# Optimization experiments

Measured on AMD Instinct MI355X. Metric: run time of the kernel, lower is better.

Reference implementation:

```python
import jax, jax.numpy as jnp
import numpy as np

NQ = 4  # n_qubits_per_head


def _apply_ry(state, theta, q):
    # state: (N, 2,2,2,2) real amplitudes; theta: (N,) per-element angle; wire q
    st = jnp.moveaxis(state, 1 + q, -1)
    c = jnp.cos(0.5 * theta).reshape(-1, 1, 1, 1)
    s = jnp.sin(0.5 * theta).reshape(-1, 1, 1, 1)
    a0, a1 = st[..., 0], st[..., 1]
    st = jnp.stack([c * a0 - s * a1, s * a0 + c * a1], axis=-1)
    return jnp.moveaxis(st, -1, 1 + q)


def _apply_cnot(state, ctrl, tgt):
    st = jnp.moveaxis(state, (1 + ctrl, 1 + tgt), (-2, -1))
    st = jnp.stack([st[..., 0, :], st[..., 1, ::-1]], axis=-2)
    return jnp.moveaxis(st, (-2, -1), (1 + ctrl, 1 + tgt))


def _quantum_circuit(x_in, par):
    # x_in: (N, NQ) data angles; par: (N, L, NQ) variational angles (per head, tiled)
    N = x_in.shape[0]
    L = par.shape[1]
    state = jnp.zeros((N, 2, 2, 2, 2), x_in.dtype).at[:, 0, 0, 0, 0].set(1.0)
    for l in range(L):
        for q in range(NQ):
            state = _apply_ry(state, par[:, l, q], q)
        for q in range(NQ - 1):
            state = _apply_cnot(state, q, q + 1)
        state = _apply_cnot(state, NQ - 1, 0)
    for q in range(NQ):
        state = _apply_ry(state, x_in[:, q], q)
    p = state * state  # probabilities (real amplitudes: only RY/CNOT gates)
    zs = []
    for q in range(NQ):
        st = jnp.moveaxis(p, 1 + q, -1)
        zs.append(jnp.sum(st[..., 0], axis=(1, 2, 3)) - jnp.sum(st[..., 1], axis=(1, 2, 3)))
    return jnp.stack(zs, axis=-1)  # (N, NQ)


def setup_inputs() -> dict:
    key = jax.random.key(0)
    ks = jax.random.split(key, 6)
    B, T, E, H, L = 4, 2048, 1024, 16, 2
    scale = 1.0 / np.sqrt(E)
    x = jax.random.normal(ks[0], (B, T, E), dtype=jnp.float32)
    Wq = jax.random.normal(ks[1], (E, E), dtype=jnp.float32) * scale
    Wk = jax.random.normal(ks[2], (E, E), dtype=jnp.float32) * scale
    Wv = jax.random.normal(ks[3], (E, E), dtype=jnp.float32) * scale
    Wo = jax.random.normal(ks[4], (E, E), dtype=jnp.float32) * scale
    qparams = jax.random.normal(ks[5], (H, L, NQ), dtype=jnp.float32)
    return {"x": x, "Wq": Wq, "Wk": Wk, "Wv": Wv, "Wo": Wo, "qparams": qparams}


def reference(x, Wq, Wk, Wv, Wo, qparams):
    B, T, E = x.shape
    H, L, _ = qparams.shape
    hd = E // H
    q = x @ Wq.T
    k = x @ Wk.T
    v = x @ Wv.T
    # NOTE: original scales by sqrt(embed_dim), not sqrt(head_dim)
    scores = jnp.einsum('bte,bse->bts', q, k) / jnp.sqrt(jnp.asarray(E, x.dtype))
    w = jax.nn.softmax(scores, axis=-1)
    out = jnp.einsum('bts,bse->bte', w, v)
    oh = out.reshape(B, T, H, hd)
    N = B * T * H
    xin = oh[..., :NQ].reshape(N, NQ)
    par = jnp.broadcast_to(qparams[None, None], (B, T, H, L, NQ)).reshape(N, L, NQ)
    z = _quantum_circuit(xin, par)  # (N, NQ)
    zfull = jnp.concatenate([z, jnp.zeros((N, hd - NQ), x.dtype)], axis=-1)
    return zfull.reshape(B, T, E) @ Wo.T
```

## Files before the change

### kernel.cpp

```cpp
#include <hip/hip_runtime.h>
#include <hip/hip_fp16.h>

typedef _Float16 half_t;
typedef __attribute__((ext_vector_type(4))) _Float16 half4;
typedef __attribute__((ext_vector_type(8))) _Float16 half8;
typedef __attribute__((ext_vector_type(4))) float floatx4;

__device__ __forceinline__ void async_copy16(const void* src, void* dst_lds) {
  __builtin_amdgcn_global_load_lds(
      (__attribute__((address_space(1))) void*)src,
      (__attribute__((address_space(3))) void*)dst_lds, 16, 0, 0);
}

__global__ __launch_bounds__(512, 2) void gemm_nt_256(
    const half_t* __restrict__ A, const half_t* __restrict__ B,
    half_t* __restrict__ C,
    int lda, int ldb, int ldc, int kIters,
    long sAz2, long sBz2, long sCz2, float scale)
{
  __shared__ __align__(16) half_t sm[2][2][256 * 64];

  const int tid  = threadIdx.x;
  const int wave = tid >> 6, lane = tid & 63;
  const int wm = wave >> 2, wn = wave & 3;
  const int er = lane >> 4, ec = lane & 15;
  const int sw = ec & 7;

  const long z = blockIdx.z;
  const half_t* Ab = A + (long)blockIdx.x * 256 * lda + z * sAz2;
  const half_t* Bb = B + (long)blockIdx.y * 256 * ldb + z * sBz2;

  const int srow = tid >> 3;
  const int skq  = (tid & 7) ^ (srow & 7);

  floatx4 acc[2][2][4][2];
  #pragma unroll
  for (int a = 0; a < 2; a++)
    #pragma unroll
    for (int b = 0; b < 2; b++)
      #pragma unroll
      for (int i = 0; i < 4; i++)
        #pragma unroll
        for (int j = 0; j < 2; j++)
          acc[a][b][i][j] = (floatx4){0.f, 0.f, 0.f, 0.f};

#define STAGE_A(bb, hf, kt) do {                                              \
    const half_t* Ak_ = Ab + (long)(kt) * 64;                                 \
    _Pragma("unroll")                                                         \
    for (int r_ = 0; r_ < 2; r_++) {                                          \
      int lrow_ = r_ * 64 + srow;                                             \
      async_copy16(Ak_ + (long)((hf) * 128 + lrow_) * lda + skq * 8,          \
                   &sm[(bb)][0][(hf) * 8192 + (r_ * 512 + wave * 64) * 8]);   \
    } } while (0)

#define STAGE_B(bb, hf, kt) do {                                              \
    const half_t* Bk_ = Bb + (long)(kt) * 64;                                 \
    _Pragma("unroll")                                                         \
    for (int r_ = 0; r_ < 2; r_++) {                                          \
      int lrow_ = r_ * 64 + srow;                                             \
      async_copy16(Bk_ + (long)((hf) * 128 + lrow_) * ldb + skq * 8,          \
                   &sm[(bb)][1][(hf) * 8192 + (r_ * 512 + wave * 64) * 8]);   \
    } } while (0)

#define DS_A(DST, BB, MH) do {                                                \
    _Pragma("unroll")                                                         \
    for (int ii = 0; ii < 4; ii++) {                                          \
      int row_ = (MH) * 128 + wm * 64 + ii * 16 + ec;                         \
      _Pragma("unroll")                                                       \
      for (int ks = 0; ks < 2; ks++)                                          \
        DST[ii][ks] = *(const half8*)                                         \
            &sm[BB][0][row_ * 64 + (((ks * 4 + er) ^ sw) * 8)];               \
    } } while (0)

#define DS_B(DST, BB, NH) do {                                                \
    _Pragma("unroll")                                                         \
    for (int jj = 0; jj < 2; jj++) {                                          \
      int row_ = (NH) * 128 + wn * 32 + jj * 16 + ec;                         \
      _Pragma("unroll")                                                       \
      for (int ks = 0; ks < 2; ks++)                                          \
        DST[jj][ks] = *(const half8*)                                         \
            &sm[BB][1][row_ * 64 + (((ks * 4 + er) ^ sw) * 8)];               \
    } } while (0)

#define MFMA_Q(AF, BF, MH, NH) do {                                           \
    __builtin_amdgcn_s_setprio(1);                                            \
    _Pragma("unroll")                                                         \
    for (int ks = 0; ks < 2; ks++)                                            \
      _Pragma("unroll")                                                       \
      for (int ii = 0; ii < 4; ii++)                                          \
        _Pragma("unroll")                                                     \
        for (int jj = 0; jj < 2; jj++)                                        \
          acc[MH][NH][ii][jj] = __builtin_amdgcn_mfma_f32_16x16x32_f16(       \
              AF[ii][ks], BF[jj][ks], acc[MH][NH][ii][jj], 0, 0, 0);          \
    __builtin_amdgcn_s_setprio(0);                                            \
  } while (0)

#define BAR() __builtin_amdgcn_s_barrier()
#define LGKM0() do { asm volatile("s_waitcnt lgkmcnt(0)" ::: "memory");       \
                     __builtin_amdgcn_sched_barrier(0); } while (0)
#define VMW(N) asm volatile("s_waitcnt vmcnt(" #N ")" ::: "memory")

  half8 afX[4][2], bfX[2][2], bfY[2][2];
  int cur = 0;
  const int nt = kIters;

  STAGE_A(0, 0, 0); STAGE_B(0, 0, 0); STAGE_B(0, 1, 0); STAGE_A(0, 1, 0);
  VMW(4);
  BAR();

  for (int n = 0; n < nt; ++n) {
    const int hasNext = (n + 1 < nt);
    DS_A(afX, cur, 0);
    DS_B(bfX, cur, 0);
    if (hasNext) STAGE_A(cur ^ 1, 0, n + 1);
    BAR(); LGKM0();
    MFMA_Q(afX, bfX, 0, 0);
    if (hasNext) { VMW(4); } else { VMW(0); }
    BAR();
    DS_B(bfY, cur, 1);
    if (hasNext) STAGE_B(cur ^ 1, 0, n + 1);
    BAR(); LGKM0();
    MFMA_Q(afX, bfY, 0, 1);
    if (hasNext) VMW(4);
    BAR();
    DS_A(afX, cur, 1);
    if (hasNext) STAGE_B(cur ^ 1, 1, n + 1);
    BAR(); LGKM0();
    MFMA_Q(afX, bfY, 1, 1);
    BAR();
    if (hasNext) STAGE_A(cur ^ 1, 1, n + 1);
    MFMA_Q(afX, bfX, 1, 0);
    if (hasNext) VMW(4);
    BAR();
    cur ^= 1;
  }

#undef STAGE_A
#undef STAGE_B
#undef DS_A
#undef DS_B
#undef MFMA_Q
#undef BAR
#undef LGKM0
#undef VMW

  const long rowBase = (long)blockIdx.x * 256;
  const long colBase = (long)blockIdx.y * 256;
  half_t* Cz = C + z * sCz2;
  #pragma unroll
  for (int mh = 0; mh < 2; mh++)
    #pragma unroll
    for (int nh = 0; nh < 2; nh++)
      #pragma unroll
      for (int ii = 0; ii < 4; ii++)
        #pragma unroll
        for (int jj = 0; jj < 2; jj++)
          #pragma unroll
          for (int r = 0; r < 4; r++) {
            long row = rowBase + mh * 128 + wm * 64 + ii * 16 + er * 4 + r;
            long col = colBase + nh * 128 + wn * 32 + jj * 16 + ec;
            Cz[row * (long)ldc + col] =
                (_Float16)(acc[mh][nh][ii][jj][r] * scale);
          }
}

template<int BN, int EPI>
__global__ __launch_bounds__(256) void gemm_nt(
    const half_t* __restrict__ A, const half_t* __restrict__ B,
    void* __restrict__ Cout,
    int lda, int ldb, int ldc, int kIters, int zShift,
    long sAz1, long sBz1, long sCz1,
    long sAz2, long sBz2, long sCz2, float scale,
    const float* __restrict__ qab)
{
  constexpr int BM = 128;
  constexpr int WN = BN / 2;
  constexpr int AN = WN / 16;
  constexpr int RA = BM * 8 / 256;
  constexpr int RB = BN * 8 / 256;
  __shared__ __align__(16) half_t lA[BM * 64];
  __shared__ __align__(16) half_t lB[BN * 64];

  const int tid  = threadIdx.x;
  const int wave = tid >> 6, lane = tid & 63;
  const int wm = wave >> 1, wn = wave & 1;
  const int er = lane >> 4, ec = lane & 15;
  const int sw = ec & 7;

  const long z = blockIdx.z;
  const long z2 = z >> zShift;
  const long z1 = z - (z2 << zShift);
  const half_t* Ab = A + (long)blockIdx.x * BM * lda + z1 * sAz1 + z2 * sAz2;
  const half_t* Bb = B + (long)blockIdx.y * BN * ldb + z1 * sBz1 + z2 * sBz2;
  const long cz = z1 * sCz1 + z2 * sCz2;

  floatx4 acc[4][AN];
  #pragma unroll
  for (int i = 0; i < 4; i++)
    #pragma unroll
    for (int j = 0; j < AN; j++)
      acc[i][j] = (floatx4){0.f, 0.f, 0.f, 0.f};

  for (int ks = 0; ks < kIters; ++ks) {
    const half_t* Ak = Ab + ks * 64;
    const half_t* Bk = Bb + ks * 64;
    #pragma unroll
    for (int r = 0; r < RA; r++) {
      int s = r * 256 + tid;
      int row = s >> 3;
      int kq = (s & 7) ^ (row & 7);
      async_copy16(Ak + (long)row * lda + kq * 8,
                   &lA[(r * 256 + wave * 64) * 8]);
    }
    #pragma unroll
    for (int r = 0; r < RB; r++) {
      int s = r * 256 + tid;
      int row = s >> 3;
      int kq = (s & 7) ^ (row & 7);
      async_copy16(Bk + (long)row * ldb + kq * 8,
                   &lB[(r * 256 + wave * 64) * 8]);
    }
    __syncthreads();

    #pragma unroll
    for (int h = 0; h < 2; h++) {
      half8 af[4], bfv[AN];
      #pragma unroll
      for (int i = 0; i < 4; i++) {
        int row = wm * 64 + i * 16 + ec;
        af[i] = *(const half8*)&lA[row * 64 + (((h * 4 + er) ^ sw) * 8)];
      }
      #pragma unroll
      for (int j = 0; j < AN; j++) {
        int row = wn * WN + j * 16 + ec;
        bfv[j] = *(const half8*)&lB[row * 64 + (((h * 4 + er) ^ sw) * 8)];
      }
      #pragma unroll
      for (int i = 0; i < 4; i++)
        #pragma unroll
        for (int j = 0; j < AN; j++)
          acc[i][j] = __builtin_amdgcn_mfma_f32_16x16x32_f16(
              af[i], bfv[j], acc[i][j], 0, 0, 0);
    }
    __syncthreads();
  }

  const long rowBase = (long)blockIdx.x * BM + wm * 64;
  const long colBase = (long)blockIdx.y * BN + wn * WN;
  #pragma unroll
  for (int i = 0; i < 4; i++)
    #pragma unroll
    for (int j = 0; j < AN; j++)
      #pragma unroll
      for (int r = 0; r < 4; r++) {
        long row = rowBase + i * 16 + er * 4 + r;
        long col = colBase + j * 16 + ec;
        float v = acc[i][j][r];
        if constexpr (EPI == 0) {
          ((half_t*)Cout)[cz + row * (long)ldc + col] = (_Float16)(v * scale);
        } else if constexpr (EPI == 1) {
          ((half_t*)Cout)[cz + col * (long)ldc + row] = (_Float16)v;
        } else if constexpr (EPI == 2) {
          ((float*)Cout)[cz + row * (long)ldc + col] = v * scale;
        } else if constexpr (EPI == 4) {
          ((float*)Cout)[cz + col * (long)ldc + row] = v;
        } else {
          float za = qab[2 * (int)col], zb = qab[2 * (int)col + 1];
          float zv = za * cosf(v) + zb * sinf(v);
          ((half_t*)Cout)[cz + row * (long)ldc + col] = (_Float16)zv;
        }
      }
}

__global__ __launch_bounds__(256) void pv_softmax(
    const half_t* __restrict__ S, const half_t* __restrict__ V,
    float* __restrict__ Op, float* __restrict__ Lp, int kIters)
{
  __shared__ __align__(16) half_t lA[128 * 64];
  __shared__ __align__(16) half_t lB[64 * 64];

  const int tid  = threadIdx.x;
  const int wave = tid >> 6, lane = tid & 63;
  const int wm = wave >> 1, wn = wave & 1;
  const int er = lane >> 4, ec = lane & 15;
  const int sw = ec & 7;

  const long z = blockIdx.z;
  const long z2 = z >> 2;
  const long z1 = z & 3;
  const half_t* Ab = S + (long)blockIdx.x * 128 * 2048
                       + z1 * ((long)2048 * 2048) + z2 * 512;
  const half_t* Bb = V + z1 * 2048 + z2 * 512;

  floatx4 acc[4][2];
  #pragma unroll
  for (int i = 0; i < 4; i++)
    #pragma unroll
    for (int j = 0; j < 2; j++)
      acc[i][j] = (floatx4){0.f, 0.f, 0.f, 0.f};
  float lsum[4] = {0.f, 0.f, 0.f, 0.f};

  for (int ks = 0; ks < kIters; ++ks) {
    const half_t* Ak = Ab + ks * 64;
    const half_t* Bk = Bb + ks * 64;
    #pragma unroll
    for (int r = 0; r < 4; r++) {
      int s = r * 256 + tid;
      int row = s >> 3;
      int kq = (s & 7) ^ (row & 7);
      async_copy16(Ak + (long)row * 2048 + kq * 8,
                   &lA[(r * 256 + wave * 64) * 8]);
    }
    #pragma unroll
    for (int r = 0; r < 2; r++) {
      int s = r * 256 + tid;
      int row = s >> 3;
      int kq = (s & 7) ^ (row & 7);
      async_copy16(Bk + (long)row * 8192 + kq * 8,
                   &lB[(r * 256 + wave * 64) * 8]);
    }
    __syncthreads();

    #pragma unroll
    for (int h = 0; h < 2; h++) {
      half8 af[4], bfv[2];
      #pragma unroll
      for (int i = 0; i < 4; i++) {
        int row = wm * 64 + i * 16 + ec;
        half8 a = *(const half8*)&lA[row * 64 + (((h * 4 + er) ^ sw) * 8)];
        #pragma unroll
        for (int k = 0; k < 8; k++) {
          float e = __expf((float)a[k]);
          _Float16 ph = (_Float16)e;
          a[k] = ph;
          lsum[i] += (float)ph;
        }
        af[i] = a;
      }
      #pragma unroll
      for (int j = 0; j < 2; j++) {
        int row = wn * 32 + j * 16 + ec;
        bfv[j] = *(const half8*)&lB[row * 64 + (((h * 4 + er) ^ sw) * 8)];
      }
      #pragma unroll
      for (int i = 0; i < 4; i++)
        #pragma unroll
        for (int j = 0; j < 2; j++)
          acc[i][j] = __builtin_amdgcn_mfma_f32_16x16x32_f16(
              af[i], bfv[j], acc[i][j], 0, 0, 0);
    }
    __syncthreads();
  }

  const long zo = z2 * ((long)8192 * 64) + z1 * ((long)2048 * 64);
  const long rowBase = (long)blockIdx.x * 128 + wm * 64;
  #pragma unroll
  for (int i = 0; i < 4; i++)
    #pragma unroll
    for (int j = 0; j < 2; j++)
      #pragma unroll
      for (int r = 0; r < 4; r++) {
        long row = rowBase + i * 16 + er * 4 + r;
        long col = wn * 32 + j * 16 + ec;
        Op[zo + row * 64 + col] = acc[i][j][r];
      }

  const long lb = z2 * 8192 + z1 * 2048 + (long)blockIdx.x * 128 + wm * 64;
  #pragma unroll
  for (int i = 0; i < 4; i++) {
    float v = lsum[i];
    v += __shfl_xor(v, 16);
    v += __shfl_xor(v, 32);
    if (wn == 0 && er == 0) Lp[lb + i * 16 + ec] = v;
  }
}

__global__ __launch_bounds__(256) void v4_reduce(const float* __restrict__ P,
                                                 half_t* __restrict__ O)
{
  const long CH = (long)64 * 8192;
  long i = ((long)blockIdx.x * 256 + threadIdx.x) * 4;
  float4 a = *(const float4*)(P + i);
  float4 b = *(const float4*)(P + i + CH);
  float4 c = *(const float4*)(P + i + 2 * CH);
  float4 d = *(const float4*)(P + i + 3 * CH);
  half4 o;
  o[0] = (_Float16)(a.x + b.x + c.x + d.x);
  o[1] = (_Float16)(a.y + b.y + c.y + d.y);
  o[2] = (_Float16)(a.z + b.z + c.z + d.z);
  o[3] = (_Float16)(a.w + b.w + c.w + d.w);
  *(half4*)(O + i) = o;
}

__global__ __launch_bounds__(256) void z_reduce_quantum(
    const float* __restrict__ P, const float* __restrict__ Lp,
    const float* __restrict__ qab, half_t* __restrict__ O)
{
  const long CH = (long)8192 * 64;
  long i = ((long)blockIdx.x * 256 + threadIdx.x) * 4;
  long t = i >> 6;
  float4 a = *(const float4*)(P + i);
  float4 b = *(const float4*)(P + i + CH);
  float4 c = *(const float4*)(P + i + 2 * CH);
  float4 d = *(const float4*)(P + i + 3 * CH);
  float l = Lp[t] + Lp[8192 + t] + Lp[2 * 8192 + t] + Lp[3 * 8192 + t];
  float inv = 1.f / l;
  float s[4] = {(a.x + b.x + c.x + d.x) * inv, (a.y + b.y + c.y + d.y) * inv,
                (a.z + b.z + c.z + d.z) * inv, (a.w + b.w + c.w + d.w) * inv};
  int c0 = (int)(i & 63);
  half4 o;
  #pragma unroll
  for (int j = 0; j < 4; j++) {
    float za = qab[2 * (c0 + j)], zb = qab[2 * (c0 + j) + 1];
    o[j] = (_Float16)(za * cosf(s[j]) + zb * sinf(s[j]));
  }
  *(half4*)(O + i) = o;
}

__global__ __launch_bounds__(256) void softmax_rows(half_t* __restrict__ S,
                                                    int ld)
{
  const long row = blockIdx.x;
  half8* sp = (half8*)(S + row * (long)ld);
  const int t = threadIdx.x;
  const int wave = t >> 6, lane = t & 63;
  half8 hv = sp[t];
  float e[8];
  #pragma unroll
  for (int k = 0; k < 8; k++) e[k] = (float)hv[k];
  float m = e[0];
  #pragma unroll
  for (int k = 1; k < 8; k++) m = fmaxf(m, e[k]);
  #pragma unroll
  for (int o = 32; o > 0; o >>= 1) m = fmaxf(m, __shfl_xor(m, o));
  __shared__ float rmax[4], rsum[4];
  if (lane == 0) rmax[wave] = m;
  __syncthreads();
  m = fmaxf(fmaxf(rmax[0], rmax[1]), fmaxf(rmax[2], rmax[3]));
  float s = 0.f;
  #pragma unroll
  for (int k = 0; k < 8; k++) { e[k] = expf(e[k] - m); s += e[k]; }
  #pragma unroll
  for (int o = 32; o > 0; o >>= 1) s += __shfl_xor(s, o);
  if (lane == 0) rsum[wave] = s;
  __syncthreads();
  float inv = 1.f / (rsum[0] + rsum[1] + rsum[2] + rsum[3]);
  half8 o8;
  #pragma unroll
  for (int k = 0; k < 8; k++) o8[k] = (_Float16)(e[k] * inv);
  sp[t] = o8;
}

__global__ __launch_bounds__(256) void prep_all(
    const float* __restrict__ x,  const float* __restrict__ Wq,
    const float* __restrict__ Wk, const float* __restrict__ Wv,
    const float* __restrict__ Wo, const float* __restrict__ qp, int L,
    half_t* __restrict__ xh, half_t* __restrict__ Wqk,
    half_t* __restrict__ Wv4, half_t* __restrict__ Wos,
    float* __restrict__ qab)
{
  const int bid = blockIdx.x;
  if (bid < 4096) {
    long i = ((long)bid * 256 + threadIdx.x) * 8;
    float4 a = *(const float4*)(x + i);
    float4 b = *(const float4*)(x + i + 4);
    half8 h = {(_Float16)a.x, (_Float16)a.y, (_Float16)a.z, (_Float16)a.w,
               (_Float16)b.x, (_Float16)b.y, (_Float16)b.z, (_Float16)b.w};
    *(half8*)(xh + i) = h;
  } else if (bid < 5120) {
    long i = ((long)(bid - 4096) * 256 + threadIdx.x) * 8;
    int r = (int)(i >> 10);
    int e = (int)(i & 1023);
    const float* src = (r < 1024 ? Wq + (long)r * 1024
                                 : Wk + (long)(r - 1024) * 1024) + e;
    float4 a = *(const float4*)src;
    float4 b = *(const float4*)(src + 4);
    half8 h = {(_Float16)a.x, (_Float16)a.y, (_Float16)a.z, (_Float16)a.w,
               (_Float16)b.x, (_Float16)b.y, (_Float16)b.z, (_Float16)b.w};
    *(half8*)(Wqk + i) = h;
  } else if (bid < 5152) {
    long i = ((long)(bid - 5120) * 256 + threadIdx.x) * 8;
    int c = (int)(i >> 10);
    int e = (int)(i & 1023);
    const float* src = Wv + (long)(((c >> 2) << 6) | (c & 3)) * 1024 + e;
    float4 a = *(const float4*)src;
    float4 b = *(const float4*)(src + 4);
    half8 h = {(_Float16)a.x, (_Float16)a.y, (_Float16)a.z, (_Float16)a.w,
               (_Float16)b.x, (_Float16)b.y, (_Float16)b.z, (_Float16)b.w};
    *(half8*)(Wv4 + i) = h;
  } else if (bid < 5408) {
    int idx = (bid - 5152) * 256 + threadIdx.x;
    int e = idx >> 6, c = idx & 63;
    Wos[idx] = (_Float16)Wo[(long)e * 1024 + (((c >> 2) << 6) | (c & 3))];
  } else {
    int h = threadIdx.x;
    if (h >= 16) return;
    float st[16];
    #pragma unroll
    for (int i = 0; i < 16; i++) st[i] = 0.f;
    st[0] = 1.f;
    for (int l = 0; l < L; l++) {
      #pragma unroll
      for (int q = 0; q < 4; q++) {
        float th = qp[(h * L + l) * 4 + q];
        float c = cosf(0.5f * th), s = sinf(0.5f * th);
        int mq = 8 >> q;
        #pragma unroll
        for (int i = 0; i < 16; i++) {
          if ((i & mq) == 0) {
            float a0 = st[i], a1 = st[i | mq];
            st[i]      = c * a0 - s * a1;
            st[i | mq] = s * a0 + c * a1;
          }
        }
      }
      const int cm[4] = {8, 4, 2, 1};
      const int tm[4] = {4, 2, 1, 8};
      #pragma unroll
      for (int p = 0; p < 4; p++) {
        int mc = cm[p], mt = tm[p];
        #pragma unroll
        for (int i = 0; i < 16; i++) {
          if ((i & mc) != 0 && (i & mt) == 0) {
            float tv = st[i]; st[i] = st[i | mt]; st[i | mt] = tv;
          }
        }
      }
    }
    #pragma unroll
    for (int q = 0; q < 4; q++) {
      int mq = 8 >> q;
      float zc = 0.f, xc = 0.f;
      #pragma unroll
      for (int i = 0; i < 16; i++) {
        float p2 = st[i] * st[i];
        zc += ((i & mq) == 0) ? p2 : -p2;
        if ((i & mq) == 0) xc += st[i] * st[i | mq];
      }
      qab[(h * 4 + q) * 2 + 0] = zc;
      qab[(h * 4 + q) * 2 + 1] = -2.f * xc;
    }
  }
}

extern "C" void kernel_launch(void* const* d_in, const int* in_sizes, int n_in,
                              void* d_out, int out_size, void* d_ws, size_t ws_size,
                              hipStream_t stream)
{
  const float* x  = (const float*)d_in[0];
  const float* Wq = (const float*)d_in[1];
  const float* Wk = (const float*)d_in[2];
  const float* Wv = (const float*)d_in[3];
  const float* Wo = (const float*)d_in[4];
  const float* qp = (const float*)d_in[5];
  const int L = in_sizes[5] / 64;
  float* out = (float*)d_out;

  char* w = (char*)d_ws;
  size_t off = 0;
  auto alloc = [&](size_t bytes) -> void* {
    void* p = w + off;
    off = (off + bytes + 255) & ~(size_t)255;
    return p;
  };
  float*  qab  = (float*)alloc(512);
  half_t* xh   = (half_t*)alloc((size_t)8192 * 1024 * 2);
  half_t* Wqk  = (half_t*)alloc((size_t)2048 * 1024 * 2);
  half_t* Wv4  = (half_t*)alloc((size_t)64 * 1024 * 2);
  half_t* Wos  = (half_t*)alloc((size_t)1024 * 64 * 2);
  half_t* V4th = (half_t*)alloc((size_t)64 * 8192 * 2);
  half_t* Z4   = (half_t*)alloc((size_t)8192 * 64 * 2);
  float*  Lp   = (float*)alloc((size_t)4 * 8192 * 4);

  half_t* QKb = (half_t*)d_out;

  int tier = (ws_size >= off + (size_t)8192 * 2048 * 2 + 256) ? 0 : 1;
  const size_t Sn = (tier == 0) ? (size_t)8192 * 2048 : (size_t)2048 * 2048;
  half_t* S = (half_t*)alloc(Sn * 2);

  prep_all<<<dim3(5409), dim3(256), 0, stream>>>(
      x, Wq, Wk, Wv, Wo, qp, L, xh, Wqk, Wv4, Wos, qab);

  gemm_nt_256<<<dim3(32, 8, 1), 512, 0, stream>>>(
      xh, Wqk, QKb, 1024, 1024, 2048, 16, 0, 0, 0, 1.f);

  if (tier == 0) {
    float* V4p = (float*)S;
    gemm_nt<64, 4><<<dim3(64, 1, 4), 256, 0, stream>>>(
        xh, Wv4, V4p, 1024, 1024, 8192, 4, 0,
        0, 0, 0, 256, 256, (long)64 * 8192, 1.f, nullptr);
    v4_reduce<<<dim3(512), dim3(256), 0, stream>>>(V4p, V4th);

    gemm_nt_256<<<dim3(8, 8, 4), 512, 0, stream>>>(
        QKb, QKb + 1024, S, 2048, 2048, 2048, 16,
        (long)2048 * 2048, (long)2048 * 2048, (long)2048 * 2048, 0.03125f);

    float* Zp = (float*)d_out;
    pv_softmax<<<dim3(16, 1, 16), 256, 0, stream>>>(S, V4th, Zp, Lp, 8);
    z_reduce_quantum<<<dim3(512), dim3(256), 0, stream>>>(Zp, Lp, qab, Z4);
  } else {
    gemm_nt<64, 1><<<dim3(64, 1, 1), 256, 0, stream>>>(
        xh, Wv4, V4th, 1024, 1024, 8192, 16, 0,
        0, 0, 0, 0, 0, 0, 1.f, nullptr);
    for (int b = 0; b < 4; b++) {
      const long q0 = (long)b * 2048;
      gemm_nt<128, 0><<<dim3(16, 16, 1), 256, 0, stream>>>(
          QKb + q0 * 2048, QKb + 1024 + q0 * 2048, S,
          2048, 2048, 2048, 16, 0, 0, 0, 0, 0, 0, 0, 0.03125f, nullptr);
      softmax_rows<<<dim3(2048), dim3(256), 0, stream>>>(S, 2048);
      gemm_nt<64, 5><<<dim3(16, 1, 1), 256, 0, stream>>>(
          S, V4th + q0, Z4 + q0 * 64, 2048, 8192, 64, 32, 0,
          0, 0, 0, 0, 0, 0, 1.f, qab);
    }
  }

  gemm_nt<128, 2><<<dim3(64, 8, 1), 256, 0, stream>>>(
      Z4, Wos, out, 64, 64, 1024, 1, 0,
      0, 0, 0, 0, 0, 0, 1.f, nullptr);
}
```

Before: 211.8 us.

## Deepen GEMM prefetch pipeline by unrolling main loop two K-tiles per iteration

Restructures the GEMM main loop to process two K-tiles per iteration with static buffer indices. More global-to-LDS stages are kept in flight (vmcnt waits of 6 instead of 4), and the per-quarter vmcnt waits inside a tile are removed so loads overlap more of the MFMA work. This assumes kIters is even; an odd count would silently drop the last tile. It also makes the waits more complex to reason about for correctness.

Result: no change. 211.3 us (-0.3%).

```diff
diff --git a/kernel.cpp b/kernel.cpp
--- a/kernel.cpp
+++ b/kernel.cpp
@@ -101,38 +101,54 @@
 #define VMW(N) asm volatile("s_waitcnt vmcnt(" #N ")" ::: "memory")
 
   half8 afX[4][2], bfX[2][2], bfY[2][2];
-  int cur = 0;
   const int nt = kIters;
 
   STAGE_A(0, 0, 0); STAGE_B(0, 0, 0); STAGE_B(0, 1, 0); STAGE_A(0, 1, 0);
-  VMW(4);
+  STAGE_A(1, 0, 1); STAGE_B(1, 0, 1); STAGE_B(1, 1, 1);
+  VMW(6);
   BAR();
 
-  for (int n = 0; n < nt; ++n) {
-    const int hasNext = (n + 1 < nt);
-    DS_A(afX, cur, 0);
-    DS_B(bfX, cur, 0);
-    if (hasNext) STAGE_A(cur ^ 1, 0, n + 1);
+  for (int i = 0; i < nt / 2; ++i) {
+    const int u = 2 * i, vtl = 2 * i + 1;
+    const int nx = (u + 2 < nt);
+    DS_A(afX, 0, 0); DS_B(bfX, 0, 0);
+    STAGE_A(1, 1, vtl);
     BAR(); LGKM0();
     MFMA_Q(afX, bfX, 0, 0);
-    if (hasNext) { VMW(4); } else { VMW(0); }
-    BAR();
-    DS_B(bfY, cur, 1);
-    if (hasNext) STAGE_B(cur ^ 1, 0, n + 1);
+    BAR();
+    DS_B(bfY, 0, 1);
+    if (nx) STAGE_A(0, 0, u + 2);
     BAR(); LGKM0();
     MFMA_Q(afX, bfY, 0, 1);
-    if (hasNext) VMW(4);
-    BAR();
-    DS_A(afX, cur, 1);
-    if (hasNext) STAGE_B(cur ^ 1, 1, n + 1);
+    BAR();
+    DS_A(afX, 0, 1);
+    if (nx) STAGE_B(0, 0, u + 2);
     BAR(); LGKM0();
     MFMA_Q(afX, bfY, 1, 1);
     BAR();
-    if (hasNext) STAGE_A(cur ^ 1, 1, n + 1);
+    if (nx) STAGE_B(0, 1, u + 2);
     MFMA_Q(afX, bfX, 1, 0);
-    if (hasNext) VMW(4);
-    BAR();
-    cur ^= 1;
+    if (nx) { VMW(6); } else { VMW(0); }
+    BAR();
+    DS_A(afX, 1, 0); DS_B(bfX, 1, 0);
+    if (nx) STAGE_A(0, 1, u + 2);
+    BAR(); LGKM0();
+    MFMA_Q(afX, bfX, 0, 0);
+    BAR();
+    DS_B(bfY, 1, 1);
+    if (nx) STAGE_A(1, 0, u + 3);
+    BAR(); LGKM0();
+    MFMA_Q(afX, bfY, 0, 1);
+    BAR();
+    DS_A(afX, 1, 1);
+    if (nx) STAGE_B(1, 0, u + 3);
+    BAR(); LGKM0();
+    MFMA_Q(afX, bfY, 1, 1);
+    BAR();
+    if (nx) STAGE_B(1, 1, u + 3);
+    MFMA_Q(afX, bfX, 1, 0);
+    if (nx) { VMW(6); } else { VMW(0); }
+    BAR();
   }
 
 #undef STAGE_A
```
